# Kernel tuning notes

Measured on AMD Instinct MI355X. Metric: run time of the kernel, lower is better.

Reference implementation:

```python
import jax, jax.numpy as jnp
import numpy as np

DIM = 384
H = 12
HD = DIM // H  # 32
GROUPS = 6
K = 7
EPS = 1e-5


def layernorm(x, g, b):
    m = x.mean(-1, keepdims=True)
    v = x.var(-1, keepdims=True)
    return (x - m) * jax.lax.rsqrt(v + EPS) * g + b


def setup_inputs() -> dict:
    key = jax.random.key(0)
    ks = jax.random.split(key, 12)
    B, S = 8, 4096
    s = 0.02
    inp = {
        "x": jax.random.normal(ks[0], (B, S, DIM), jnp.float32),
        # grouped Conv1d: weight (out=384, in_per_group=64, k=7)
        "conv_w": jax.random.normal(ks[1], (DIM, DIM // GROUPS, K), jnp.float32) * s,
        "conv_b": jnp.zeros((DIM,), jnp.float32),
        "q_w": jax.random.normal(ks[2], (DIM, DIM), jnp.float32) * s,
        "q_b": jnp.zeros((DIM,), jnp.float32),
        "k_w": jax.random.normal(ks[3], (DIM, DIM), jnp.float32) * s,
        "k_b": jnp.zeros((DIM,), jnp.float32),
        "v_w": jax.random.normal(ks[4], (DIM, DIM), jnp.float32) * s,
        "v_b": jnp.zeros((DIM,), jnp.float32),
        "g_w": jax.random.normal(ks[5], (DIM, DIM), jnp.float32) * s,
        "g_b": jnp.zeros((DIM,), jnp.float32),
        "decay": jnp.ones((1, H, 1, HD), jnp.float32) * 0.85,
        "ln1_g": jnp.ones((DIM,), jnp.float32),
        "ln1_b": jnp.zeros((DIM,), jnp.float32),
        "w1": jax.random.normal(ks[6], (DIM, 2 * DIM), jnp.float32) * s,
        "b1": jnp.zeros((2 * DIM,), jnp.float32),
        "w2": jax.random.normal(ks[7], (2 * DIM, DIM), jnp.float32) * s,
        "b2": jnp.zeros((DIM,), jnp.float32),
        "ln2_g": jnp.ones((DIM,), jnp.float32),
        "ln2_b": jnp.zeros((DIM,), jnp.float32),
    }
    return inp


def reference(x, conv_w, conv_b, q_w, q_b, k_w, k_b, v_w, v_b, g_w, g_b,
              decay, ln1_g, ln1_b, w1, b1, w2, b2, ln2_g, ln2_b):
    b, s, d = x.shape
    # grouped depth-blocked conv over time (torch Conv1d, pad=3, groups=6)
    xc = jax.lax.conv_general_dilated(
        x.transpose(0, 2, 1), conv_w, window_strides=(1,), padding=((3, 3),),
        feature_group_count=GROUPS, dimension_numbers=("NCH", "OIH", "NCH"))
    xc = (xc + conv_b[None, :, None]).transpose(0, 2, 1)
    xc = jax.nn.silu(xc)

    def heads(y):  # (b,s,d) -> (b,h,s,hd)
        return y.reshape(b, s, H, HD).transpose(0, 2, 1, 3)

    q = heads(xc @ q_w + q_b)
    k = heads(xc @ k_w + k_b)
    v = heads(xc @ v_w + v_b)
    g = heads(jax.nn.sigmoid(xc @ g_w + g_b))
    v_gated = v * g

    # Fallback recurrence: state = state * mean(sigmoid(decay)) + v_t (x) k_t;
    # output reads only diag(state) -> collapses to a per-dim decayed cumsum of v*k.
    lam = jnp.mean(jax.nn.sigmoid(decay))  # scalar (mean over h,d of expanded w)
    u = v_gated * k                        # (b,h,s,hd)
    u_t = u.transpose(2, 0, 1, 3)          # (s,b,h,hd)

    def step(carry, ut):
        c = carry * lam + ut
        return c, c

    _, diag = jax.lax.scan(step, jnp.zeros((b, H, HD), x.dtype), u_t)
    out = q * diag.transpose(1, 2, 0, 3)   # (b,h,s,hd)

    x_mem = out.transpose(0, 2, 1, 3).reshape(b, s, d)
    h = layernorm(x_mem, ln1_g, ln1_b)
    h = jax.nn.silu(h @ w1 + b1) @ w2 + b2
    return layernorm(h + x, ln2_g, ln2_b)
```

## Files before the change

kernel.cpp:

```cpp
#include <hip/hip_runtime.h>
#include <hip/hip_bf16.h>

#define DIMD 384
#define SEQL 4096
#define NBATCH 8
#define NTOK (NBATCH*SEQL)

typedef float f32x4 __attribute__((ext_vector_type(4)));
typedef short s16x8 __attribute__((ext_vector_type(8)));
typedef unsigned short u16;
typedef __hip_bfloat16 bf16;

__device__ __forceinline__ float sigf(float x){ return 1.f/(1.f+__expf(-x)); }

typedef __attribute__((address_space(3))) void lds_void;
typedef const __attribute__((address_space(1))) void glb_void;
__device__ __forceinline__ void gl_lds16(const void* g, void* l) {
  __builtin_amdgcn_global_load_lds((glb_void*)g, (lds_void*)l, 16, 0, 0);
}

#define OFF_LAM   0ul
#define OFF_WQ    4096ul
#define OFF_CW    (OFF_WQ + 1179648ul)
#define OFF_W1T   (OFF_CW + 344064ul)
#define OFF_W2T   (OFF_W1T + 589824ul)
#define OFF_XC    4194304ul
#define OFF_Q     (OFF_XC + 25165824ul)
#define OFF_U     (OFF_XC + 50331648ul)
#define OFF_AI    OFF_U
#define OFF_H     (OFF_U + 50331648ul)

__global__ void k_prep_w(const float* __restrict__ qw, const float* __restrict__ kw,
                         const float* __restrict__ vw, const float* __restrict__ gw,
                         const float* __restrict__ cw, const float* __restrict__ w1,
                         const float* __restrict__ w2,
                         bf16* __restrict__ wqt, bf16* __restrict__ cwt,
                         bf16* __restrict__ w1t, bf16* __restrict__ w2t) {
  const int total = 589824 + 172032 + 294912 + 294912;
  for (int j = blockIdx.x*blockDim.x + threadIdx.x; j < total; j += gridDim.x*blockDim.x) {
    if (j < 589824) {
      int n = j / 384, k = j % 384;
      int mat = n / 384;
      int np = n % 384;
      const float* W = (mat==0)?qw:(mat==1)?kw:(mat==2)?vw:gw;
      wqt[(size_t)n*384 + k] = __float2bfloat16(W[(size_t)k*384 + np]);
    } else if (j < 589824 + 172032) {
      int jj = j - 589824;
      int o = jj / 448, k = jj % 448;
      int kap = k >> 6, i = k & 63;
      cwt[(size_t)o*448 + k] = __float2bfloat16(cw[((size_t)o*64 + i)*7 + kap]);
    } else if (j < 589824 + 172032 + 294912) {
      int jj = j - (589824 + 172032);
      int n = jj / 384, k = jj % 384;
      w1t[(size_t)n*384 + k] = __float2bfloat16(w1[(size_t)k*768 + n]);
    } else {
      int jj = j - (589824 + 172032 + 294912);
      int n = jj / 768, k = jj % 768;
      w2t[(size_t)n*768 + k] = __float2bfloat16(w2[(size_t)k*384 + n]);
    }
  }
}

__global__ void k_prep_lam(const float* __restrict__ decay, float* __restrict__ lam) {
  __shared__ float red[6];
  int t = threadIdx.x;
  float v = sigf(decay[t]);
  for (int off = 32; off; off >>= 1) v += __shfl_xor(v, off, 64);
  if ((t & 63) == 0) red[t >> 6] = v;
  __syncthreads();
  if (t == 0) {
    float s = 0.f;
    for (int i = 0; i < 6; ++i) s += red[i];
    lam[0] = s * (1.f/384.f);
  }
}

__global__ __launch_bounds__(256) void k_conv(const float* __restrict__ x, const float* __restrict__ cb,
                                              const bf16* __restrict__ cwt, bf16* __restrict__ xc) {
  int id = blockIdx.x;
  int g = id % 6, st = (id/6) & 31, b = id / 192;
  int s0 = st * 128;
  __shared__ u16 xls[134*72];
  __shared__ u16 wls[64*456];
  int tid = threadIdx.x;
  for (int r0 = 0; r0 < 144; r0 += 16) {
    int row = r0 + (tid >> 4);
    if (row < 134) {
      int col = (tid & 15) * 4;
      int s = s0 - 3 + row;
      float4 v = make_float4(0.f,0.f,0.f,0.f);
      if (s >= 0 && s < SEQL)
        v = *reinterpret_cast<const float4*>(x + ((size_t)(b*SEQL + s))*DIMD + g*64 + col);
      u16* dst = &xls[row*72 + col];
      bf16 t0 = __float2bfloat16(v.x); dst[0] = *reinterpret_cast<u16*>(&t0);
      bf16 t1 = __float2bfloat16(v.y); dst[1] = *reinterpret_cast<u16*>(&t1);
      bf16 t2 = __float2bfloat16(v.z); dst[2] = *reinterpret_cast<u16*>(&t2);
      bf16 t3 = __float2bfloat16(v.w); dst[3] = *reinterpret_cast<u16*>(&t3);
    }
  }
  for (int i0 = 0; i0 < 28672; i0 += 1024) {
    int i = i0 + tid*4;
    int o = i / 448, k = i % 448;
    *reinterpret_cast<uint2*>(&wls[o*456 + k]) =
      *reinterpret_cast<const uint2*>(cwt + ((size_t)(g*64 + o))*448 + k);
  }
  __syncthreads();
  int w = tid >> 6, l = tid & 63, l15 = l & 15, lh = l >> 4;
  f32x4 zz = {0.f,0.f,0.f,0.f};
  f32x4 acc[2][4];
  for (int i=0;i<2;++i) for (int jn=0;jn<4;++jn) acc[i][jn]=zz;
  for (int kap = 0; kap < 7; ++kap) {
#pragma unroll
    for (int ic = 0; ic < 2; ++ic) {
      s16x8 a0 = *reinterpret_cast<const s16x8*>(&xls[(w*32 +  0 + l15 + kap)*72 + ic*32 + lh*8]);
      s16x8 a1 = *reinterpret_cast<const s16x8*>(&xls[(w*32 + 16 + l15 + kap)*72 + ic*32 + lh*8]);
#pragma unroll
      for (int nf = 0; nf < 4; ++nf) {
        s16x8 bfr = *reinterpret_cast<const s16x8*>(&wls[(nf*16 + l15)*456 + kap*64 + ic*32 + lh*8]);
        acc[0][nf] = __builtin_amdgcn_mfma_f32_16x16x32_bf16(a0, bfr, acc[0][nf], 0,0,0);
        acc[1][nf] = __builtin_amdgcn_mfma_f32_16x16x32_bf16(a1, bfr, acc[1][nf], 0,0,0);
      }
    }
  }
#pragma unroll
  for (int nf = 0; nf < 4; ++nf) {
    int ch = g*64 + nf*16 + l15;
    float bias = cb[ch];
#pragma unroll
    for (int mf = 0; mf < 2; ++mf) {
#pragma unroll
      for (int r = 0; r < 4; ++r) {
        int m = w*32 + mf*16 + lh*4 + r;
        float v = acc[mf][nf][r] + bias;
        v = v * sigf(v);
        xc[((size_t)(b*SEQL + s0 + m))*DIMD + ch] = __float2bfloat16(v);
      }
    }
  }
}

__global__ __launch_bounds__(256) void k_qkvg(const bf16* __restrict__ xc, const bf16* __restrict__ wt,
    const float* __restrict__ qb, const float* __restrict__ kb,
    const float* __restrict__ vb, const float* __restrict__ gb,
    bf16* __restrict__ qout, bf16* __restrict__ uout) {
  int raw = blockIdx.x;
  int vv = (raw & 7)*384 + (raw >> 3);
  int mt = vv / 12, ct = vv % 12;
  int m0 = mt*128, c0 = ct*32;
  __shared__ __align__(16) u16 smem[16384];
  u16* als = smem;
  int tid = threadIdx.x, w = tid >> 6, l = tid & 63, l15 = l & 15, lh = l >> 4;
  f32x4 zz = {0.f,0.f,0.f,0.f};
  f32x4 acc[8][2];
#pragma unroll
  for (int i=0;i<8;++i){ acc[i][0]=zz; acc[i][1]=zz; }
  const bf16* b0p = wt + ((size_t)(w*384 + c0 + l15))*384 + lh*8;
  const bf16* b1p = b0p + (size_t)16*384;
  s16x8 c0A = *reinterpret_cast<const s16x8*>(b0p);
  s16x8 c1A = *reinterpret_cast<const s16x8*>(b1p);
  s16x8 c0B, c1B;
  for (int kc = 0; kc < 3; ++kc) {
#pragma unroll
    for (int p = 0; p < 8; ++p) {
      int off16 = p*256 + tid;
      int row = off16 >> 4, slot = off16 & 15;
      int sslot = slot ^ (row & 7);
      gl_lds16(xc + ((size_t)(m0+row))*DIMD + kc*128 + sslot*8,
               (char*)als + off16*16);
    }
    __syncthreads();
#pragma unroll
    for (int kk = 0; kk < 4; ++kk) {
      s16x8 cur0 = (kk & 1) ? c0B : c0A;
      s16x8 cur1 = (kk & 1) ? c1B : c1A;
      int nko = (kk < 3) ? (kc*128 + (kk+1)*32) : ((kc < 2) ? (kc+1)*128 : -1);
      if (nko >= 0) {
        if (kk & 1) { c0A = *reinterpret_cast<const s16x8*>(b0p + nko);
                      c1A = *reinterpret_cast<const s16x8*>(b1p + nko); }
        else        { c0B = *reinterpret_cast<const s16x8*>(b0p + nko);
                      c1B = *reinterpret_cast<const s16x8*>(b1p + nko); }
      }
#pragma unroll
      for (int mf = 0; mf < 8; ++mf) {
        s16x8 af = *reinterpret_cast<const s16x8*>(
            &als[(mf*16 + l15)*128 + (((kk*4 + lh) ^ (l15 & 7))*8)]);
        acc[mf][0] = __builtin_amdgcn_mfma_f32_16x16x32_bf16(af, cur0, acc[mf][0], 0,0,0);
        acc[mf][1] = __builtin_amdgcn_mfma_f32_16x16x32_bf16(af, cur1, acc[mf][1], 0,0,0);
      }
    }
    __syncthreads();
  }
  const float* bp = (w==0)?qb:(w==1)?kb:(w==2)?vb:gb;
  float bias0 = bp[c0 + l15], bias1 = bp[c0 + 16 + l15];
  if (w == 0) {
#pragma unroll
    for (int mf=0;mf<8;++mf)
#pragma unroll
      for (int nf=0;nf<2;++nf) {
        float bs = nf ? bias1 : bias0;
#pragma unroll
        for (int r=0;r<4;++r) {
          int m = mf*16 + lh*4 + r, c = nf*16 + l15;
          qout[((size_t)(m0+m))*DIMD + c0 + c] = __float2bfloat16(acc[mf][nf][r] + bs);
        }
      }
  } else {
    u16* exm = smem + (size_t)(w-1)*(128*40);
#pragma unroll
    for (int mf=0;mf<8;++mf)
#pragma unroll
      for (int nf=0;nf<2;++nf) {
        float bs = nf ? bias1 : bias0;
#pragma unroll
        for (int r=0;r<4;++r) {
          int m = mf*16 + lh*4 + r, c = nf*16 + l15;
          bf16 t = __float2bfloat16(acc[mf][nf][r] + bs);
          exm[m*40 + c] = *reinterpret_cast<u16*>(&t);
        }
      }
  }
  __syncthreads();
#pragma unroll
  for (int p = 0; p < 16; ++p) {
    int idx = p*256 + tid;
    int m = idx >> 5, c = idx & 31;
    u16 kr = smem[0*(128*40) + m*40 + c];
    u16 vr = smem[1*(128*40) + m*40 + c];
    u16 gr = smem[2*(128*40) + m*40 + c];
    float kvv = __bfloat162float(*reinterpret_cast<bf16*>(&kr));
    float vvv = __bfloat162float(*reinterpret_cast<bf16*>(&vr));
    float gvv = __bfloat162float(*reinterpret_cast<bf16*>(&gr));
    uout[((size_t)(m0+m))*DIMD + c0 + c] = __float2bfloat16(vvv * sigf(gvv) * kvv);
  }
}

__global__ __launch_bounds__(384) void k_scan(const bf16* __restrict__ u, const bf16* __restrict__ q,
    const float* __restrict__ lam_p, const float* __restrict__ l1g, const float* __restrict__ l1b,
    bf16* __restrict__ h) {
  int b = blockIdx.x >> 5, c = blockIdx.x & 31;
  int d = threadIdx.x;
  float lam = lam_p[0];
  __shared__ float ols[32*384];
  __shared__ float lgs[384], lbs[384];
  lgs[d] = l1g[d]; lbs[d] = l1b[d];
  int s0 = c*128;
  size_t base = ((size_t)b*SEQL)*DIMD + d;
  float carry = 0.f;
  int sstart = s0 - 64; if (sstart < 0) sstart = 0;
  for (int s = sstart; s < s0; s += 8) {
    float uv[8];
#pragma unroll
    for (int j = 0; j < 8; ++j) uv[j] = __bfloat162float(u[base + (size_t)(s+j)*DIMD]);
#pragma unroll
    for (int j = 0; j < 8; ++j) carry = carry*lam + uv[j];
  }
  int w = d >> 6, lane = d & 63;
  for (int p = 0; p < 4; ++p) {
    int sb = s0 + p*32;
    __syncthreads();
    for (int it0 = 0; it0 < 32; it0 += 8) {
      float uv[8], qv[8];
#pragma unroll
      for (int j = 0; j < 8; ++j) uv[j] = __bfloat162float(u[base + (size_t)(sb+it0+j)*DIMD]);
#pragma unroll
      for (int j = 0; j < 8; ++j) qv[j] = __bfloat162float(q[base + (size_t)(sb+it0+j)*DIMD]);
#pragma unroll
      for (int j = 0; j < 8; ++j) {
        carry = carry*lam + uv[j];
        ols[(it0+j)*384 + d] = carry * qv[j];
      }
    }
    __syncthreads();
    for (int t = w; t < 32; t += 6) {
      float vv[6]; float s1 = 0.f, s2 = 0.f;
#pragma unroll
      for (int j = 0; j < 6; ++j) {
        vv[j] = ols[t*384 + j*64 + lane];
        s1 += vv[j]; s2 += vv[j]*vv[j];
      }
      for (int off = 32; off; off >>= 1) { s1 += __shfl_xor(s1, off, 64); s2 += __shfl_xor(s2, off, 64); }
      float mean = s1 * (1.f/384.f);
      float var = s2 * (1.f/384.f) - mean*mean;
      float rs = rsqrtf(var + 1e-5f);
      size_t rowo = ((size_t)(b*SEQL + sb + t))*DIMD;
#pragma unroll
      for (int j = 0; j < 6; ++j) {
        int dd = j*64 + lane;
        h[rowo + dd] = __float2bfloat16((vv[j]-mean)*rs*lgs[dd] + lbs[dd]);
      }
    }
  }
}

__global__ __launch_bounds__(256) void k_mlp1(const bf16* __restrict__ h, const bf16* __restrict__ w1t,
                                              const float* __restrict__ b1, bf16* __restrict__ ai) {
  int raw = blockIdx.x;
  int vv = (raw & 7)*192 + (raw >> 3);
  int mt = vv / 6, nt = vv % 6;
  int m0 = mt*128, n0 = nt*128;
  __shared__ __align__(16) u16 als[16384];
  int tid = threadIdx.x, w = tid >> 6, l = tid & 63, l15 = l & 15, lh = l >> 4;
  int wm = (w >> 1)*64, wn = (w & 1)*64;
  f32x4 zz = {0.f,0.f,0.f,0.f};
  f32x4 acc[4][4];
#pragma unroll
  for (int i=0;i<4;++i) for (int jn=0;jn<4;++jn) acc[i][jn]=zz;
  const bf16* bp0 = w1t + ((size_t)(n0 + wn + l15))*384 + lh*8;
  s16x8 bA[4], bB[4];
#pragma unroll
  for (int nf = 0; nf < 4; ++nf)
    bA[nf] = *reinterpret_cast<const s16x8*>(bp0 + (size_t)nf*16*384);
  for (int kc = 0; kc < 3; ++kc) {
#pragma unroll
    for (int p = 0; p < 8; ++p) {
      int off16 = p*256 + tid;
      int row = off16 >> 4, slot = off16 & 15;
      int sslot = slot ^ (row & 7);
      gl_lds16(h + ((size_t)(m0+row))*DIMD + kc*128 + sslot*8,
               (char*)als + off16*16);
    }
    __syncthreads();
#pragma unroll
    for (int kk = 0; kk < 4; ++kk) {
      int nko = (kk < 3) ? (kc*128 + (kk+1)*32) : ((kc < 2) ? (kc+1)*128 : -1);
      if (nko >= 0) {
        if (kk & 1) {
#pragma unroll
          for (int nf = 0; nf < 4; ++nf)
            bA[nf] = *reinterpret_cast<const s16x8*>(bp0 + (size_t)nf*16*384 + nko);
        } else {
#pragma unroll
          for (int nf = 0; nf < 4; ++nf)
            bB[nf] = *reinterpret_cast<const s16x8*>(bp0 + (size_t)nf*16*384 + nko);
        }
      }
#pragma unroll
      for (int mf = 0; mf < 4; ++mf) {
        s16x8 af = *reinterpret_cast<const s16x8*>(
            &als[(wm + mf*16 + l15)*128 + (((kk*4 + lh) ^ (l15 & 7))*8)]);
#pragma unroll
        for (int nf = 0; nf < 4; ++nf)
          acc[mf][nf] = __builtin_amdgcn_mfma_f32_16x16x32_bf16(
              af, (kk & 1) ? bB[nf] : bA[nf], acc[mf][nf], 0,0,0);
      }
    }
    __syncthreads();
  }
  float bias[4];
#pragma unroll
  for (int nf = 0; nf < 4; ++nf) bias[nf] = b1[n0 + wn + nf*16 + l15];
#pragma unroll
  for (int mf = 0; mf < 4; ++mf)
#pragma unroll
    for (int nf = 0; nf < 4; ++nf)
#pragma unroll
      for (int r = 0; r < 4; ++r) {
        int m = wm + mf*16 + lh*4 + r, ch = n0 + wn + nf*16 + l15;
        float v = acc[mf][nf][r] + bias[nf];
        v = v * sigf(v);
        ai[(size_t)(m0+m)*768 + ch] = __float2bfloat16(v);
      }
}

__global__ __launch_bounds__(512) void k_mlp2ln(const bf16* __restrict__ ai, const bf16* __restrict__ w2t,
                                                const float* __restrict__ b2, const float* __restrict__ x,
                                                const float* __restrict__ l2g, const float* __restrict__ l2b,
                                                float* __restrict__ out) {
  int raw = blockIdx.x;
  int mt = (raw & 7)*64 + (raw >> 3);
  int m0 = mt*64;
  __shared__ __align__(16) u16 als[8192];
  __shared__ float pls[8][64][2];
  int tid = threadIdx.x, w = tid >> 6, l = tid & 63, l15 = l & 15, lh = l >> 4;
  int wn = w*48;
  f32x4 zz = {0.f,0.f,0.f,0.f};
  f32x4 acc[4][3];
#pragma unroll
  for (int i=0;i<4;++i)
#pragma unroll
    for (int jn=0;jn<3;++jn) acc[i][jn]=zz;
  const bf16* bp0 = w2t + ((size_t)(wn + l15))*768 + lh*8;
  s16x8 bA[3], bB[3];
#pragma unroll
  for (int nf = 0; nf < 3; ++nf)
    bA[nf] = *reinterpret_cast<const s16x8*>(bp0 + (size_t)nf*16*768);
  for (int kc = 0; kc < 6; ++kc) {
#pragma unroll
    for (int p = 0; p < 2; ++p) {
      int off16 = p*512 + tid;
      int row = off16 >> 4, slot = off16 & 15;
      int sslot = slot ^ (row & 7);
      gl_lds16(ai + ((size_t)(m0+row))*768 + kc*128 + sslot*8,
               (char*)als + off16*16);
    }
    __syncthreads();
#pragma unroll
    for (int kk = 0; kk < 4; ++kk) {
      int nko = (kk < 3) ? (kc*128 + (kk+1)*32) : ((kc < 5) ? (kc+1)*128 : -1);
      if (nko >= 0) {
        if (kk & 1) {
#pragma unroll
          for (int nf = 0; nf < 3; ++nf)
            bA[nf] = *reinterpret_cast<const s16x8*>(bp0 + (size_t)nf*16*768 + nko);
        } else {
#pragma unroll
          for (int nf = 0; nf < 3; ++nf)
            bB[nf] = *reinterpret_cast<const s16x8*>(bp0 + (size_t)nf*16*768 + nko);
        }
      }
#pragma unroll
      for (int mf = 0; mf < 4; ++mf) {
        s16x8 af = *reinterpret_cast<const s16x8*>(
            &als[(mf*16 + l15)*128 + (((kk*4 + lh) ^ (l15 & 7))*8)]);
#pragma unroll
        for (int nf = 0; nf < 3; ++nf)
          acc[mf][nf] = __builtin_amdgcn_mfma_f32_16x16x32_bf16(
              af, (kk & 1) ? bB[nf] : bA[nf], acc[mf][nf], 0,0,0);
      }
    }
    __syncthreads();
  }
  float bias[3];
#pragma unroll
  for (int nf = 0; nf < 3; ++nf) bias[nf] = b2[wn + nf*16 + l15];
#pragma unroll
  for (int mf = 0; mf < 4; ++mf) {
#pragma unroll
    for (int r = 0; r < 4; ++r) {
      int m = mf*16 + lh*4 + r;
      const float* xr = x + (size_t)(m0+m)*DIMD + wn + l15;
      float sa = 0.f, sb = 0.f;
#pragma unroll
      for (int nf = 0; nf < 3; ++nf) {
        float v = acc[mf][nf][r] + bias[nf] + xr[nf*16];
        acc[mf][nf][r] = v;
        sa += v; sb += v*v;
      }
#pragma unroll
      for (int off = 1; off < 16; off <<= 1) {
        sa += __shfl_xor(sa, off, 16);
        sb += __shfl_xor(sb, off, 16);
      }
      if (l15 == 0) { pls[w][m][0] = sa; pls[w][m][1] = sb; }
    }
  }
  __syncthreads();
  float lg[3], lb[3];
#pragma unroll
  for (int nf = 0; nf < 3; ++nf) { lg[nf] = l2g[wn + nf*16 + l15]; lb[nf] = l2b[wn + nf*16 + l15]; }
#pragma unroll
  for (int mf = 0; mf < 4; ++mf) {
#pragma unroll
    for (int r = 0; r < 4; ++r) {
      int m = mf*16 + lh*4 + r;
      float S1 = 0.f, S2 = 0.f;
#pragma unroll
      for (int ww = 0; ww < 8; ++ww) { S1 += pls[ww][m][0]; S2 += pls[ww][m][1]; }
      float mean = S1 * (1.f/384.f);
      float var = S2 * (1.f/384.f) - mean*mean;
      float rs = rsqrtf(var + 1e-5f);
      float* orow = out + (size_t)(m0+m)*DIMD + wn + l15;
#pragma unroll
      for (int nf = 0; nf < 3; ++nf)
        orow[nf*16] = (acc[mf][nf][r] - mean)*rs*lg[nf] + lb[nf];
    }
  }
}

extern "C" void kernel_launch(void* const* d_in, const int* in_sizes, int n_in,
                              void* d_out, int out_size, void* d_ws, size_t ws_size,
                              hipStream_t stream) {
  const float* x   = (const float*)d_in[0];
  const float* cw  = (const float*)d_in[1];
  const float* cb  = (const float*)d_in[2];
  const float* qw  = (const float*)d_in[3];
  const float* qb  = (const float*)d_in[4];
  const float* kw  = (const float*)d_in[5];
  const float* kb  = (const float*)d_in[6];
  const float* vw  = (const float*)d_in[7];
  const float* vb  = (const float*)d_in[8];
  const float* gw  = (const float*)d_in[9];
  const float* gb  = (const float*)d_in[10];
  const float* dec = (const float*)d_in[11];
  const float* l1g = (const float*)d_in[12];
  const float* l1b = (const float*)d_in[13];
  const float* w1  = (const float*)d_in[14];
  const float* b1  = (const float*)d_in[15];
  const float* w2  = (const float*)d_in[16];
  const float* b2  = (const float*)d_in[17];
  const float* l2g = (const float*)d_in[18];
  const float* l2b = (const float*)d_in[19];

  char* ws = (char*)d_ws;
  float* lam = (float*)(ws + OFF_LAM);
  bf16* wqt  = (bf16*)(ws + OFF_WQ);
  bf16* cwt  = (bf16*)(ws + OFF_CW);
  bf16* w1t  = (bf16*)(ws + OFF_W1T);
  bf16* w2t  = (bf16*)(ws + OFF_W2T);
  bf16* xc   = (bf16*)(ws + OFF_XC);
  bf16* q    = (bf16*)(ws + OFF_Q);
  bf16* u    = (bf16*)(ws + OFF_U);
  bf16* hbuf = (bf16*)(ws + OFF_H);
  bf16* ai   = (bf16*)(ws + OFF_AI);
  float* out = (float*)d_out;

  hipLaunchKernelGGL(k_prep_w,  dim3(1024), dim3(256), 0, stream, qw,kw,vw,gw,cw,w1,w2, wqt,cwt,w1t,w2t);
  hipLaunchKernelGGL(k_prep_lam,dim3(1),    dim3(384), 0, stream, dec, lam);
  hipLaunchKernelGGL(k_conv,    dim3(1536), dim3(256), 0, stream, x, cb, cwt, xc);
  hipLaunchKernelGGL(k_qkvg,    dim3(3072), dim3(256), 0, stream, xc, wqt, qb,kb,vb,gb, q, u);
  hipLaunchKernelGGL(k_scan,    dim3(256),  dim3(384), 0, stream, u, q, lam, l1g, l1b, hbuf);
  hipLaunchKernelGGL(k_mlp1,    dim3(1536), dim3(256), 0, stream, hbuf, w1t, b1, ai);
  hipLaunchKernelGGL(k_mlp2ln,  dim3(512),  dim3(512), 0, stream, ai, w2t, b2, x, l2g, l2b, out);
}
```

Baseline: 243.5 us.

## Split qkvg GEMM by rows per wave, fusing gating in registers

Each wave in the q/k/v/g projection kernel previously computed one of the four projections over all 128 rows. It now computes all four projections for its own 32-row slice, so q, k, v and g for a given element sit in one thread's registers. The v*sigmoid(g)*k gating is then done directly in the epilogue, which removes the LDS exchange buffers and the extra barrier. In exchange, each wave loads eight B fragments per k-step straight from global memory with no double-buffered prefetch, which adds load latency and register pressure.

```diff
diff --git a/kernel.cpp b/kernel.cpp
--- a/kernel.cpp
+++ b/kernel.cpp
@@ -147,18 +147,16 @@
   int vv = (raw & 7)*384 + (raw >> 3);
   int mt = vv / 12, ct = vv % 12;
   int m0 = mt*128, c0 = ct*32;
-  __shared__ __align__(16) u16 smem[16384];
-  u16* als = smem;
+  __shared__ __align__(16) u16 als[16384];
   int tid = threadIdx.x, w = tid >> 6, l = tid & 63, l15 = l & 15, lh = l >> 4;
+  int wm = w*32;
   f32x4 zz = {0.f,0.f,0.f,0.f};
-  f32x4 acc[8][2];
-#pragma unroll
-  for (int i=0;i<8;++i){ acc[i][0]=zz; acc[i][1]=zz; }
-  const bf16* b0p = wt + ((size_t)(w*384 + c0 + l15))*384 + lh*8;
-  const bf16* b1p = b0p + (size_t)16*384;
-  s16x8 c0A = *reinterpret_cast<const s16x8*>(b0p);
-  s16x8 c1A = *reinterpret_cast<const s16x8*>(b1p);
-  s16x8 c0B, c1B;
+  f32x4 acc[2][8];
+#pragma unroll
+  for (int i=0;i<2;++i)
+#pragma unroll
+    for (int j=0;j<8;++j) acc[i][j]=zz;
+  const bf16* bbase = wt + ((size_t)(c0 + l15))*384 + lh*8;
   for (int kc = 0; kc < 3; ++kc) {
 #pragma unroll
     for (int p = 0; p < 8; ++p) {
@@ -171,66 +169,47 @@
     __syncthreads();
 #pragma unroll
     for (int kk = 0; kk < 4; ++kk) {
-      s16x8 cur0 = (kk & 1) ? c0B : c0A;
-      s16x8 cur1 = (kk & 1) ? c1B : c1A;
-      int nko = (kk < 3) ? (kc*128 + (kk+1)*32) : ((kc < 2) ? (kc+1)*128 : -1);
-      if (nko >= 0) {
-        if (kk & 1) { c0A = *reinterpret_cast<const s16x8*>(b0p + nko);
-                      c1A = *reinterpret_cast<const s16x8*>(b1p + nko); }
-        else        { c0B = *reinterpret_cast<const s16x8*>(b0p + nko);
-                      c1B = *reinterpret_cast<const s16x8*>(b1p + nko); }
-      }
-#pragma unroll
-      for (int mf = 0; mf < 8; ++mf) {
+      int ko = kc*128 + kk*32;
+      s16x8 bfr[8];
+#pragma unroll
+      for (int mb = 0; mb < 4; ++mb)
+#pragma unroll
+        for (int nf = 0; nf < 2; ++nf)
+          bfr[mb*2+nf] = *reinterpret_cast<const s16x8*>(
+              bbase + (size_t)(mb*384 + nf*16)*384 + ko);
+#pragma unroll
+      for (int mf = 0; mf < 2; ++mf) {
         s16x8 af = *reinterpret_cast<const s16x8*>(
-            &als[(mf*16 + l15)*128 + (((kk*4 + lh) ^ (l15 & 7))*8)]);
-        acc[mf][0] = __builtin_amdgcn_mfma_f32_16x16x32_bf16(af, cur0, acc[mf][0], 0,0,0);
-        acc[mf][1] = __builtin_amdgcn_mfma_f32_16x16x32_bf16(af, cur1, acc[mf][1], 0,0,0);
-      }
-    }
-    __syncthreads();
-  }
-  const float* bp = (w==0)?qb:(w==1)?kb:(w==2)?vb:gb;
-  float bias0 = bp[c0 + l15], bias1 = bp[c0 + 16 + l15];
-  if (w == 0) {
-#pragma unroll
-    for (int mf=0;mf<8;++mf)
-#pragma unroll
-      for (int nf=0;nf<2;++nf) {
-        float bs = nf ? bias1 : bias0;
-#pragma unroll
-        for (int r=0;r<4;++r) {
-          int m = mf*16 + lh*4 + r, c = nf*16 + l15;
-          qout[((size_t)(m0+m))*DIMD + c0 + c] = __float2bfloat16(acc[mf][nf][r] + bs);
-        }
-      }
-  } else {
-    u16* exm = smem + (size_t)(w-1)*(128*40);
-#pragma unroll
-    for (int mf=0;mf<8;++mf)
-#pragma unroll
-      for (int nf=0;nf<2;++nf) {
-        float bs = nf ? bias1 : bias0;
-#pragma unroll
-        for (int r=0;r<4;++r) {
-          int m = mf*16 + lh*4 + r, c = nf*16 + l15;
-          bf16 t = __float2bfloat16(acc[mf][nf][r] + bs);
-          exm[m*40 + c] = *reinterpret_cast<u16*>(&t);
-        }
-      }
-  }
-  __syncthreads();
-#pragma unroll
-  for (int p = 0; p < 16; ++p) {
-    int idx = p*256 + tid;
-    int m = idx >> 5, c = idx & 31;
-    u16 kr = smem[0*(128*40) + m*40 + c];
-    u16 vr = smem[1*(128*40) + m*40 + c];
-    u16 gr = smem[2*(128*40) + m*40 + c];
-    float kvv = __bfloat162float(*reinterpret_cast<bf16*>(&kr));
-    float vvv = __bfloat162float(*reinterpret_cast<bf16*>(&vr));
-    float gvv = __bfloat162float(*reinterpret_cast<bf16*>(&gr));
-    uout[((size_t)(m0+m))*DIMD + c0 + c] = __float2bfloat16(vvv * sigf(gvv) * kvv);
+            &als[(wm + mf*16 + l15)*128 + (((kk*4 + lh) ^ (l15 & 7))*8)]);
+#pragma unroll
+        for (int j = 0; j < 8; ++j)
+          acc[mf][j] = __builtin_amdgcn_mfma_f32_16x16x32_bf16(af, bfr[j], acc[mf][j], 0,0,0);
+      }
+    }
+    __syncthreads();
+  }
+  float qb0[2], kb0[2], vb0[2], gb0[2];
+#pragma unroll
+  for (int nf = 0; nf < 2; ++nf) {
+    int c = c0 + nf*16 + l15;
+    qb0[nf] = qb[c]; kb0[nf] = kb[c]; vb0[nf] = vb[c]; gb0[nf] = gb[c];
+  }
+#pragma unroll
+  for (int mf = 0; mf < 2; ++mf) {
+#pragma unroll
+    for (int nf = 0; nf < 2; ++nf) {
+#pragma unroll
+      for (int r = 0; r < 4; ++r) {
+        int m = m0 + wm + mf*16 + lh*4 + r;
+        int c = c0 + nf*16 + l15;
+        size_t idx = (size_t)m*DIMD + c;
+        qout[idx] = __float2bfloat16(acc[mf][0+nf][r] + qb0[nf]);
+        float kv = acc[mf][2+nf][r] + kb0[nf];
+        float vv2 = acc[mf][4+nf][r] + vb0[nf];
+        float gv = acc[mf][6+nf][r] + gb0[nf];
+        uout[idx] = __float2bfloat16(vv2 * sigf(gv) * kv);
+      }
+    }
   }
 }
 
```

Result: slower. 323.7 us (+32.9%).
